# Optimization experiments

Hardware: AMD Instinct MI355X
Metric: run time of the kernel (lower is better)

## Reference

```python
import jax, jax.numpy as jnp
import numpy as np

N_HEADS = 8

def setup_inputs() -> dict:
    key = jax.random.key(0)
    ks = jax.random.split(key, 7)
    B, S, D = 4, 2048, 512
    s = 1.0 / np.sqrt(D)
    return {
        "input_Q": jax.random.normal(ks[0], (B, S, D), jnp.float32),
        "input_K": jax.random.normal(ks[1], (B, S, D), jnp.float32),
        "input_V": jax.random.normal(ks[2], (B, S, D), jnp.float32),
        "W_Q": jax.random.normal(ks[3], (D, D), jnp.float32) * s,
        "W_K": jax.random.normal(ks[4], (D, D), jnp.float32) * s,
        "W_V": jax.random.normal(ks[5], (D, D), jnp.float32) * s,
        "W_O": jax.random.normal(ks[6], (D, D), jnp.float32) * s,
    }

def reference(input_Q, input_K, input_V, W_Q, W_K, W_V, W_O):
    B, Sq, D = input_Q.shape
    Sk = input_K.shape[1]
    H = N_HEADS
    d_k = D // H
    # torch nn.Linear(bias=False): y = x @ W.T
    def proj(x, W):
        return (x @ W.T).reshape(B, -1, H, d_k).transpose(0, 2, 1, 3)  # [B,H,S,dk]
    Q = proj(input_Q, W_Q)
    K = proj(input_K, W_K)
    V = proj(input_V, W_V)
    scale = 1.0 / jnp.sqrt(jnp.float32(d_k))
    scores = jnp.einsum("bhqd,bhkd->bhqk", Q, K) * scale  # [B,H,Sq,Sk]
    # TriangularCausalMask: mask strict upper triangle with -inf
    causal = jnp.tril(jnp.ones((Sq, Sk), dtype=bool))
    scores = jnp.where(causal[None, None], scores, -jnp.inf)
    attn = jax.nn.softmax(scores, axis=-1)
    context = jnp.einsum("bhqk,bhkd->bhqd", attn, V)
    context = context.transpose(0, 2, 1, 3).reshape(B, Sq, D)
    return context @ W_O.T
```

## Files before the change

kernel.cpp:

```cpp
#include <hip/hip_runtime.h>
#include <hip/hip_bf16.h>
#include <math.h>

#define B_  4
#define S_  2048
#define D_  512
#define H_  8
#define DK_ 64
#define M_  (B_ * S_)

using bf16   = __bf16;
using bf16x4 = __bf16 __attribute__((ext_vector_type(4)));
using bf16x8 = __bf16 __attribute__((ext_vector_type(8)));
using f32x4  = float __attribute__((ext_vector_type(4)));

#define MFMA16(a, b, c) __builtin_amdgcn_mfma_f32_16x16x32_bf16((a), (b), (c), 0, 0, 0)
#define EXP2(x) exp2f(x)

typedef __attribute__((address_space(3))) void       lds_void;
typedef const __attribute__((address_space(1))) void gbl_void;

__device__ __forceinline__ void async16(const bf16* g, bf16* lds) {
    __builtin_amdgcn_global_load_lds((gbl_void*)g, (lds_void*)lds, 16, 0, 0);
}

__device__ __forceinline__ bf16x8 ldg8(const bf16* p) {
    return *reinterpret_cast<const bf16x8*>(p);
}

__device__ __forceinline__ size_t fragbase(int g, int k0, int kk, int t) {
    return ((((size_t)(g * 8 + k0) * 2 + kk) * 4 + t) * 64) * 8;
}

__global__ __launch_bounds__(256) void cvt_all(
    const float* __restrict__ x0, const float* __restrict__ x1, const float* __restrict__ x2,
    const float* __restrict__ w0, const float* __restrict__ w1,
    const float* __restrict__ w2, const float* __restrict__ w3,
    bf16* __restrict__ dst)
{
    const int w    = blockIdx.x * 4 + (threadIdx.x >> 6);
    const int lane = threadIdx.x & 63;
    const int lg = lane >> 4, lc = lane & 15;
    const float* src;
    int c;
    size_t dbase;
    if (w < 24576) {
        const int seg = w >> 13;
        c = w & 8191;
        src = (seg == 0) ? x0 : (seg == 1) ? x1 : x2;
        dbase = (size_t)seg << 22;
    } else {
        const int jj = w - 24576;
        const int seg = jj >> 9;
        c = jj & 511;
        src = (seg == 0) ? w0 : (seg == 1) ? w1 : (seg == 2) ? w2 : w3;
        dbase = ((size_t)3 << 22) + ((size_t)seg << 18);
    }
    const int g = c >> 6, k0 = (c >> 3) & 7, kk = (c >> 2) & 1, t = c & 3;
    const size_t soff = ((size_t)(g * 64 + t * 16 + lc) << 9) + k0 * 64 + kk * 32 + lg * 8;
    f32x4 a = *reinterpret_cast<const f32x4*>(src + soff);
    f32x4 b = *reinterpret_cast<const f32x4*>(src + soff + 4);
    bf16x8 r;
    #pragma unroll
    for (int j = 0; j < 4; ++j) { r[j] = (bf16)a[j]; r[j + 4] = (bf16)b[j]; }
    *reinterpret_cast<bf16x8*>(dst + dbase + ((size_t)c << 9) + (size_t)lane * 8) = r;
}

__global__ __launch_bounds__(256) void gemm_qkv(
    const bf16* __restrict__ Xf, const bf16* __restrict__ Wf,
    bf16* __restrict__ qkv)
{
    const int bx  = blockIdx.x;
    const int xcd = bx & 7;
    const int idx = bx >> 3;
    const int mt  = xcd + 8 * (idx & 7);
    const int rest = idx >> 3;
    const int nt  = rest & 3;
    const int z   = rest >> 2;

    const bf16* Xz = Xf + (size_t)z * M_ * D_;
    const bf16* Wz = Wf + (size_t)z * D_ * D_;
    const bool vz = (z == 2);
    const bf16* A  = vz ? Xz : Wz;
    const bf16* Bm = vz ? Wz : Xz;

    const int lane = threadIdx.x & 63;
    const int wave = threadIdx.x >> 6;
    const int lc = lane & 15;
    const int lg = lane >> 4;
    const int gA = (vz ? 2 * mt : 2 * nt) + (wave >> 1);
    const int gB = (vz ? 2 * nt : 2 * mt) + (wave & 1);

    f32x4 acc[4][4] = {};

    #pragma unroll
    for (int k0 = 0; k0 < 8; ++k0) {
        #pragma unroll
        for (int kk = 0; kk < 2; ++kk) {
            bf16x8 af[4], bfm[4];
            #pragma unroll
            for (int t = 0; t < 4; ++t)
                af[t] = ldg8(A + fragbase(gA, k0, kk, t) + (size_t)lane * 8);
            #pragma unroll
            for (int t = 0; t < 4; ++t)
                bfm[t] = ldg8(Bm + fragbase(gB, k0, kk, t) + (size_t)lane * 8);
            #pragma unroll
            for (int mi = 0; mi < 4; ++mi)
                #pragma unroll
                for (int ni = 0; ni < 4; ++ni)
                    acc[mi][ni] = MFMA16(af[mi], bfm[ni], acc[mi][ni]);
        }
    }

    if (z < 2) {
        bf16* Y = qkv + (size_t)z * M_ * D_;
        const float sc = (z == 0) ? 0.125f * 1.4426950408889634f : 1.0f;
        #pragma unroll
        for (int mi = 0; mi < 4; ++mi)
            #pragma unroll
            for (int ni = 0; ni < 4; ++ni) {
                const int d = gA * 64 + mi * 16 + lg * 4;
                const int s = gB * 64 + ni * 16 + lc;
                bf16x4 v;
                #pragma unroll
                for (int r = 0; r < 4; ++r) v[r] = (bf16)(acc[mi][ni][r] * sc);
                const size_t oidx =
                    ((((size_t)(s >> 11) * H_ + (d >> 6)) * S_
                      + (s & (S_ - 1))) << 6) + (d & 63);
                *reinterpret_cast<bf16x4*>(&Y[oidx]) = v;
            }
    } else {
        bf16* Y = qkv + (size_t)2 * M_ * D_;
        #pragma unroll
        for (int mi = 0; mi < 4; ++mi)
            #pragma unroll
            for (int ni = 0; ni < 4; ++ni) {
                const int s = gA * 64 + mi * 16 + lg * 4;
                const int d = gB * 64 + ni * 16 + lc;
                bf16x4 v;
                #pragma unroll
                for (int r = 0; r < 4; ++r) v[r] = (bf16)acc[mi][ni][r];
                const size_t oidx =
                    ((((size_t)(s >> 11)) * H_ + (d >> 6)) << 17)
                    + (size_t)(d & 63) * S_ + (s & (S_ - 1));
                *reinterpret_cast<bf16x4*>(&Y[oidx]) = v;
            }
    }
}

__global__ __launch_bounds__(256) void gemm_out(
    const bf16* __restrict__ CtxF, const bf16* __restrict__ WoF,
    float* __restrict__ out)
{
    const int bx  = blockIdx.x;
    const int xcd = bx & 7;
    const int idx = bx >> 3;
    const int mt  = xcd + 8 * (idx & 15);
    const int nt  = idx >> 4;

    const int lane = threadIdx.x & 63;
    const int wave = threadIdx.x >> 6;
    const int lc = lane & 15;
    const int lg = lane >> 4;
    const int gA = 2 * nt + (wave >> 1);
    const int tA = (wave & 1) * 2;
    const int gB = mt;

    f32x4 acc[2][4] = {};

    #pragma unroll
    for (int k0 = 0; k0 < 8; ++k0) {
        #pragma unroll
        for (int kk = 0; kk < 2; ++kk) {
            bf16x8 af[2], bfm[4];
            #pragma unroll
            for (int ai = 0; ai < 2; ++ai)
                af[ai] = ldg8(WoF + fragbase(gA, k0, kk, tA + ai) + (size_t)lane * 8);
            #pragma unroll
            for (int t = 0; t < 4; ++t)
                bfm[t] = ldg8(CtxF + fragbase(gB, k0, kk, t) + (size_t)lane * 8);
            #pragma unroll
            for (int ai = 0; ai < 2; ++ai)
                #pragma unroll
                for (int ni = 0; ni < 4; ++ni)
                    acc[ai][ni] = MFMA16(af[ai], bfm[ni], acc[ai][ni]);
        }
    }

    #pragma unroll
    for (int ai = 0; ai < 2; ++ai)
        #pragma unroll
        for (int ni = 0; ni < 4; ++ni) {
            const int d = gA * 64 + (tA + ai) * 16 + lg * 4;
            const int s = gB * 64 + ni * 16 + lc;
            *reinterpret_cast<f32x4*>(&out[(size_t)s * D_ + d]) = acc[ai][ni];
        }
}

__device__ __forceinline__ bf16x8 pfrag(const f32x4 a, const f32x4 b) {
    union U4 { bf16x4 v; unsigned int u[2]; };
    U4 pa, pb;
    #pragma unroll
    for (int r = 0; r < 4; ++r) { pa.v[r] = (bf16)a[r]; pb.v[r] = (bf16)b[r]; }
    auto r0 = __builtin_amdgcn_permlane16_swap(pa.u[0], pb.u[0], false, false);
    auto r1 = __builtin_amdgcn_permlane16_swap(pa.u[1], pb.u[1], false, false);
    union U8 { unsigned int u[4]; bf16x8 v; } out;
    out.u[0] = r0[0]; out.u[1] = r1[0]; out.u[2] = r0[1]; out.u[3] = r1[1];
    return out.v;
}

__global__ __launch_bounds__(1024, 8) void attn(
    const bf16* __restrict__ QKV, bf16* __restrict__ CtxF)
{
    const int bx = blockIdx.x;
    const int bh = (bx & 7) * 4 + ((bx >> 3) & 3);
    const int pi = bx >> 5;
    const int b = bh >> 3, h = bh & 7;
    const size_t plane = (size_t)S_ * DK_;
    const bf16* Q  = QKV + (size_t)bh * plane;
    const bf16* Kp = QKV + (size_t)(B_ * H_) * plane + (size_t)bh * plane;
    const bf16* Vt = QKV + 2 * (size_t)(B_ * H_) * plane + (size_t)bh * plane;

    const int lane = threadIdx.x & 63;
    const int wave = threadIdx.x >> 6;
    const int half = wave >> 3;
    const int w7   = wave & 7;
    const int wv   = w7 >> 1;
    const int kh   = w7 & 1;
    const int lc = lane & 15;
    const int lg = lane >> 4;
    const int sg = ((lg & 1) << 1) | (lg >> 1);
    const int mrow = wv * 16 + lc;

    __shared__ bf16 KV[4][2][64 * 64];

    const int lo = pi;
    const int hi = 31 - pi;
    const int myq = half ? lo : hi;

    const int qR = myq * 64 + mrow;
    bf16x8 qf0 = ldg8(Q + (size_t)qR * DK_ + lg * 8);
    bf16x8 qf1 = ldg8(Q + (size_t)qR * DK_ + 32 + lg * 8);

    f32x4 accO[4] = {};
    float li = 0.f;

    auto stage = [&](int n) {
        const int kn = n * 64;
        if (half == 0) {
            const int kc = (w7 >> 2) * 4 + lg;
            async16(Kp + (size_t)(kn + (w7 & 3) * 16 + lc) * DK_ + kc * 8,
                    &KV[n & 3][0][(w7 * 64 + lane) * 8]);
        } else {
            const int kcv = (w7 >> 2) * 4 + sg;
            async16(Vt + (size_t)((w7 & 3) * 16 + lc) * S_ + kn + kcv * 8,
                    &KV[n & 3][1][(w7 * 64 + lane) * 8]);
        }
    };

    stage(0); stage(1); stage(2);

    for (int j = 0; j <= hi; ++j) {
        if (j + 2 <= hi)      asm volatile("s_waitcnt vmcnt(2)" ::: "memory");
        else if (j + 1 <= hi) asm volatile("s_waitcnt vmcnt(1)" ::: "memory");
        else                  asm volatile("s_waitcnt vmcnt(0)" ::: "memory");
        __builtin_amdgcn_s_barrier();
        if (j + 3 <= hi) stage(j + 3);

        if (j <= myq) {
            const bf16* ks = KV[j & 3][0];
            const bf16* vs = KV[j & 3][1];

            bf16x8 kf0[2], kf1[2], vf[4];
            #pragma unroll
            for (int tt = 0; tt < 2; ++tt) {
                const int t = 2 * kh + tt;
                kf0[tt] = ldg8(&ks[(t * 64 + lane) * 8]);
                kf1[tt] = ldg8(&ks[(256 + t * 64 + lane) * 8]);
            }
            #pragma unroll
            for (int t = 0; t < 4; ++t)
                vf[t] = ldg8(&vs[(kh * 256 + t * 64 + lane) * 8]);

            f32x4 st[2];
            #pragma unroll
            for (int tt = 0; tt < 2; ++tt) {
                f32x4 zz = {};
                zz = MFMA16(kf0[tt], qf0, zz);
                st[tt] = MFMA16(kf1[tt], qf1, zz);
            }
            float rs = 0.f;
            if (j == myq) {
                #pragma unroll
                for (int tt = 0; tt < 2; ++tt)
                    #pragma unroll
                    for (int r = 0; r < 4; ++r) {
                        const int kl = (2 * kh + tt) * 16 + lg * 4 + r;
                        const float pv = EXP2((kl <= mrow) ? st[tt][r] : -1e30f);
                        st[tt][r] = pv;
                        rs += pv;
                    }
            } else {
                #pragma unroll
                for (int tt = 0; tt < 2; ++tt)
                    #pragma unroll
                    for (int r = 0; r < 4; ++r) {
                        const float pv = EXP2(st[tt][r]);
                        st[tt][r] = pv;
                        rs += pv;
                    }
            }
            li += rs;

            const bf16x8 p = pfrag(st[0], st[1]);

            #pragma unroll
            for (int t = 0; t < 4; ++t)
                accO[t] = MFMA16(vf[t], p, accO[t]);
        }
    }

    __syncthreads();
    float* scr = (float*)&KV[0][0][0];
    const int slot = (half * 4 + wv) * 64 + lane;
    if (kh == 1) {
        float* s = scr + (size_t)slot * 17;
        #pragma unroll
        for (int t = 0; t < 4; ++t)
            #pragma unroll
            for (int r = 0; r < 4; ++r) s[t * 4 + r] = accO[t][r];
        s[16] = li;
    }
    __syncthreads();
    if (kh == 0) {
        const float* s = scr + (size_t)slot * 17;
        #pragma unroll
        for (int t = 0; t < 4; ++t)
            #pragma unroll
            for (int r = 0; r < 4; ++r) accO[t][r] += s[t * 4 + r];
        li += s[16];
        li += __shfl_xor(li, 16); li += __shfl_xor(li, 32);
        const float rl = 1.0f / li;
        bf16* T = (bf16*)((char*)&KV[0][0][0] + 36864) + (half * 4 + wv) * 1280;

        #pragma unroll
        for (int t = 0; t < 4; ++t) {
            bf16x4 ov;
            #pragma unroll
            for (int r = 0; r < 4; ++r) ov[r] = (bf16)(accO[t][r] * rl);
            *reinterpret_cast<bf16x4*>(&T[lc * 72 + t * 16 + lg * 4]) = ov;
        }
        #pragma unroll
        for (int kk = 0; kk < 2; ++kk) {
            bf16x8 o8 = ldg8(&T[lc * 72 + kk * 32 + lg * 8]);
            *reinterpret_cast<bf16x8*>(
                &CtxF[fragbase(b * 32 + myq, h, kk, wv) + (size_t)lane * 8]) = o8;
        }
    }
}

extern "C" void kernel_launch(void* const* d_in, const int* in_sizes, int n_in,
                              void* d_out, int out_size, void* d_ws, size_t ws_size,
                              hipStream_t stream)
{
    float* out = (float*)d_out;

    bf16* Xf   = (bf16*)d_ws;
    bf16* Wf   = Xf + (size_t)3 * M_ * D_;
    bf16* qkv  = Wf + (size_t)4 * D_ * D_;
    bf16* ctxF = qkv + (size_t)3 * M_ * D_;

    cvt_all<<<6656, 256, 0, stream>>>(
        (const float*)d_in[0], (const float*)d_in[1], (const float*)d_in[2],
        (const float*)d_in[3], (const float*)d_in[4], (const float*)d_in[5],
        (const float*)d_in[6], Xf);

    gemm_qkv<<<dim3(768), 256, 0, stream>>>(Xf, Wf, qkv);
    attn<<<dim3(512), 1024, 0, stream>>>(qkv, ctxF);
    gemm_out<<<dim3(512), 256, 0, stream>>>(ctxF, Wf + (size_t)3 * D_ * D_, out);
}
```

Before: 190.6 us.

## Process both causal query tiles per wave instead of splitting across block halves

The attention block shrinks from 16 to 8 waves. Each wave now keeps two query tiles (the high and the low one of a balanced pair) and reuses each staged K/V tile for both, instead of giving each tile to a separate half of the block. Every wave issues both the K and the V async loads, and the wait counts are doubled to match. This keeps the work per wave balanced and halves the threads per block, at the cost of more registers per wave and less parallelism per block.

```diff
diff --git a/kernel.cpp b/kernel.cpp
--- a/kernel.cpp
+++ b/kernel.cpp
@@ -209,7 +209,7 @@
     return out.v;
 }
 
-__global__ __launch_bounds__(1024, 8) void attn(
+__global__ __launch_bounds__(512, 4) void attn(
     const bf16* __restrict__ QKV, bf16* __restrict__ CtxF)
 {
     const int bx = blockIdx.x;
@@ -223,10 +223,8 @@
 
     const int lane = threadIdx.x & 63;
     const int wave = threadIdx.x >> 6;
-    const int half = wave >> 3;
-    const int w7   = wave & 7;
-    const int wv   = w7 >> 1;
-    const int kh   = w7 & 1;
+    const int wv   = wave >> 1;
+    const int kh   = wave & 1;
     const int lc = lane & 15;
     const int lg = lane >> 4;
     const int sg = ((lg & 1) << 1) | (lg >> 1);
@@ -236,52 +234,53 @@
 
     const int lo = pi;
     const int hi = 31 - pi;
-    const int myq = half ? lo : hi;
-
-    const int qR = myq * 64 + mrow;
-    bf16x8 qf0 = ldg8(Q + (size_t)qR * DK_ + lg * 8);
-    bf16x8 qf1 = ldg8(Q + (size_t)qR * DK_ + 32 + lg * 8);
-
-    f32x4 accO[4] = {};
-    float li = 0.f;
-
+
+    const int qH = hi * 64 + mrow;
+    const int qL = lo * 64 + mrow;
+    bf16x8 qfH0 = ldg8(Q + (size_t)qH * DK_ + lg * 8);
+    bf16x8 qfH1 = ldg8(Q + (size_t)qH * DK_ + 32 + lg * 8);
+    bf16x8 qfL0 = ldg8(Q + (size_t)qL * DK_ + lg * 8);
+    bf16x8 qfL1 = ldg8(Q + (size_t)qL * DK_ + 32 + lg * 8);
+
+    f32x4 accH[4] = {}, accL[4] = {};
+    float liH = 0.f, liL = 0.f;
+
+    const int srow = (wave & 3) * 16 + lc;
+    const int kc   = (wave >> 2) * 4 + lg;
+    const int kcv  = (wave >> 2) * 4 + sg;
     auto stage = [&](int n) {
         const int kn = n * 64;
-        if (half == 0) {
-            const int kc = (w7 >> 2) * 4 + lg;
-            async16(Kp + (size_t)(kn + (w7 & 3) * 16 + lc) * DK_ + kc * 8,
-                    &KV[n & 3][0][(w7 * 64 + lane) * 8]);
-        } else {
-            const int kcv = (w7 >> 2) * 4 + sg;
-            async16(Vt + (size_t)((w7 & 3) * 16 + lc) * S_ + kn + kcv * 8,
-                    &KV[n & 3][1][(w7 * 64 + lane) * 8]);
-        }
+        async16(Kp + (size_t)(kn + srow) * DK_ + kc * 8,
+                &KV[n & 3][0][(wave * 64 + lane) * 8]);
+        async16(Vt + (size_t)srow * S_ + kn + kcv * 8,
+                &KV[n & 3][1][(wave * 64 + lane) * 8]);
     };
 
     stage(0); stage(1); stage(2);
 
     for (int j = 0; j <= hi; ++j) {
-        if (j + 2 <= hi)      asm volatile("s_waitcnt vmcnt(2)" ::: "memory");
-        else if (j + 1 <= hi) asm volatile("s_waitcnt vmcnt(1)" ::: "memory");
+        if (j + 2 <= hi)      asm volatile("s_waitcnt vmcnt(4)" ::: "memory");
+        else if (j + 1 <= hi) asm volatile("s_waitcnt vmcnt(2)" ::: "memory");
         else                  asm volatile("s_waitcnt vmcnt(0)" ::: "memory");
         __builtin_amdgcn_s_barrier();
         if (j + 3 <= hi) stage(j + 3);
 
-        if (j <= myq) {
-            const bf16* ks = KV[j & 3][0];
-            const bf16* vs = KV[j & 3][1];
-
-            bf16x8 kf0[2], kf1[2], vf[4];
-            #pragma unroll
-            for (int tt = 0; tt < 2; ++tt) {
-                const int t = 2 * kh + tt;
-                kf0[tt] = ldg8(&ks[(t * 64 + lane) * 8]);
-                kf1[tt] = ldg8(&ks[(256 + t * 64 + lane) * 8]);
-            }
-            #pragma unroll
-            for (int t = 0; t < 4; ++t)
-                vf[t] = ldg8(&vs[(kh * 256 + t * 64 + lane) * 8]);
-
+        const bf16* ks = KV[j & 3][0];
+        const bf16* vs = KV[j & 3][1];
+
+        bf16x8 kf0[2], kf1[2], vf[4];
+        #pragma unroll
+        for (int tt = 0; tt < 2; ++tt) {
+            const int t = 2 * kh + tt;
+            kf0[tt] = ldg8(&ks[(t * 64 + lane) * 8]);
+            kf1[tt] = ldg8(&ks[(256 + t * 64 + lane) * 8]);
+        }
+        #pragma unroll
+        for (int t = 0; t < 4; ++t)
+            vf[t] = ldg8(&vs[(kh * 256 + t * 64 + lane) * 8]);
+
+        auto step = [&](const bf16x8& qf0, const bf16x8& qf1, bool diag,
+                        f32x4* accO, float& li) {
             f32x4 st[2];
             #pragma unroll
             for (int tt = 0; tt < 2; ++tt) {
@@ -290,7 +289,7 @@
                 st[tt] = MFMA16(kf1[tt], qf1, zz);
             }
             float rs = 0.f;
-            if (j == myq) {
+            if (diag) {
                 #pragma unroll
                 for (int tt = 0; tt < 2; ++tt)
                     #pragma unroll
@@ -311,50 +310,60 @@
                     }
             }
             li += rs;
-
             const bf16x8 p = pfrag(st[0], st[1]);
-
             #pragma unroll
             for (int t = 0; t < 4; ++t)
                 accO[t] = MFMA16(vf[t], p, accO[t]);
-        }
+        };
+
+        step(qfH0, qfH1, j == hi, accH, liH);
+        if (j <= lo) step(qfL0, qfL1, j == lo, accL, liL);
     }
 
     __syncthreads();
     float* scr = (float*)&KV[0][0][0];
-    const int slot = (half * 4 + wv) * 64 + lane;
     if (kh == 1) {
-        float* s = scr + (size_t)slot * 17;
-        #pragma unroll
-        for (int t = 0; t < 4; ++t)
-            #pragma unroll
-            for (int r = 0; r < 4; ++r) s[t * 4 + r] = accO[t][r];
-        s[16] = li;
+        #pragma unroll
+        for (int tile = 0; tile < 2; ++tile) {
+            const f32x4* accO = tile ? accL : accH;
+            float* s = scr + (size_t)((tile * 4 + wv) * 64 + lane) * 17;
+            #pragma unroll
+            for (int t = 0; t < 4; ++t)
+                #pragma unroll
+                for (int r = 0; r < 4; ++r) s[t * 4 + r] = accO[t][r];
+            s[16] = tile ? liL : liH;
+        }
     }
     __syncthreads();
     if (kh == 0) {
-        const float* s = scr + (size_t)slot * 17;
-        #pragma unroll
-        for (int t = 0; t < 4; ++t)
-            #pragma unroll
-            for (int r = 0; r < 4; ++r) accO[t][r] += s[t * 4 + r];
-        li += s[16];
-        li += __shfl_xor(li, 16); li += __shfl_xor(li, 32);
-        const float rl = 1.0f / li;
-        bf16* T = (bf16*)((char*)&KV[0][0][0] + 36864) + (half * 4 + wv) * 1280;
-
-        #pragma unroll
-        for (int t = 0; t < 4; ++t) {
-            bf16x4 ov;
-            #pragma unroll
-            for (int r = 0; r < 4; ++r) ov[r] = (bf16)(accO[t][r] * rl);
-            *reinterpret_cast<bf16x4*>(&T[lc * 72 + t * 16 + lg * 4]) = ov;
-        }
-        #pragma unroll
-        for (int kk = 0; kk < 2; ++kk) {
-            bf16x8 o8 = ldg8(&T[lc * 72 + kk * 32 + lg * 8]);
-            *reinterpret_cast<bf16x8*>(
-                &CtxF[fragbase(b * 32 + myq, h, kk, wv) + (size_t)lane * 8]) = o8;
+        #pragma unroll
+        for (int tile = 0; tile < 2; ++tile) {
+            f32x4* accO = tile ? accL : accH;
+            float li = tile ? liL : liH;
+            const float* s = scr + (size_t)((tile * 4 + wv) * 64 + lane) * 17;
+            #pragma unroll
+            for (int t = 0; t < 4; ++t)
+                #pragma unroll
+                for (int r = 0; r < 4; ++r) accO[t][r] += s[t * 4 + r];
+            li += s[16];
+            li += __shfl_xor(li, 16); li += __shfl_xor(li, 32);
+            const float rl = 1.0f / li;
+            bf16* T = (bf16*)((char*)&KV[0][0][0] + 36864)
+                      + (tile * 4 + wv) * 1280;
+            #pragma unroll
+            for (int t = 0; t < 4; ++t) {
+                bf16x4 ov;
+                #pragma unroll
+                for (int r = 0; r < 4; ++r) ov[r] = (bf16)(accO[t][r] * rl);
+                *reinterpret_cast<bf16x4*>(&T[lc * 72 + t * 16 + lg * 4]) = ov;
+            }
+            const int jq = tile ? lo : hi;
+            #pragma unroll
+            for (int kk = 0; kk < 2; ++kk) {
+                bf16x8 o8 = ldg8(&T[lc * 72 + kk * 32 + lg * 8]);
+                *reinterpret_cast<bf16x8*>(
+                    &CtxF[fragbase(b * 32 + jq, h, kk, wv) + (size_t)lane * 8]) = o8;
+            }
         }
     }
 }
@@ -376,6 +385,6 @@
         (const float*)d_in[6], Xf);
 
     gemm_qkv<<<dim3(768), 256, 0, stream>>>(Xf, Wf, qkv);
-    attn<<<dim3(512), 1024, 0, stream>>>(qkv, ctxF);
+    attn<<<dim3(512), 512, 0, stream>>>(qkv, ctxF);
     gemm_out<<<dim3(512), 256, 0, stream>>>(ctxF, Wf + (size_t)3 * D_ * D_, out);
 }
```

Measured after the change: 170.0 us. 1.12x faster.
